# Kernel optimization log

Measured on AMD Instinct MI355X. Metric: run time of the kernel, lower is better.

The kernel has to match this reference:

```python
import jax, jax.numpy as jnp
import numpy as np

N_QUBITS = 10
N_LAYERS = 3
DIM = 2 ** N_QUBITS
N_ANGLES = N_LAYERS * N_QUBITS * 3


def _ring_perm(n):
    """Combined index permutation for the 'ring' CNOT sequence (q0->q1, ..., q_{n-2}->q_{n-1}, q_{n-1}->q0).
    Qubit 0 is the most significant bit, matching bin(i).zfill(n) in the original.
    Each CNOT matrix is a permutation (involution): new_state[j] = old_state[perm[j]]."""
    def cnot_perm(control, target):
        i = np.arange(2 ** n)
        ctrl = (i >> (n - 1 - control)) & 1
        return np.where(ctrl == 1, i ^ (1 << (n - 1 - target)), i)
    total = np.arange(2 ** n)
    pairs = [(q, q + 1) for q in range(n - 1)] + [(n - 1, 0)]
    for c, t in pairs:
        total = total[cnot_perm(c, t)]
    return jnp.asarray(total)

_RING = _ring_perm(N_QUBITS)


def _single_qubit_rot(angles):
    """angles: (S, n_qubits, 3) real -> (S, n_qubits, 2, 2) complex64 Rot(phi, theta, omega)."""
    phi, theta, omega = angles[..., 0], angles[..., 1], angles[..., 2]
    ct = jnp.cos(theta / 2)
    st = jnp.sin(theta / 2)
    ppo = (phi + omega) / 2
    pmo = (phi - omega) / 2
    e_m_ppo = jnp.exp(-1j * ppo)  # complex64
    e_p_ppo = jnp.exp(1j * ppo)
    e_m_pmo = jnp.exp(-1j * pmo)
    e_p_pmo = jnp.exp(1j * pmo)
    m00 = e_m_ppo * ct
    m01 = -e_p_pmo * st
    m10 = e_m_pmo * st
    m11 = e_p_ppo * ct
    S, n = angles.shape[0], angles.shape[1]
    return jnp.stack((m00, m01, m10, m11), axis=2).reshape(S, n, 2, 2)


def _system_unitary(M):
    """Batched Kronecker product over qubits: (S, n, 2, 2) -> (S, 2^n, 2^n).
    Qubit 0 is the most significant index, matching the original einsum string."""
    S = M.shape[0]
    U = M[:, 0]
    d = 2
    for q in range(1, N_QUBITS):
        U = jnp.einsum('aij,akl->aikjl', U, M[:, q]).reshape(S, d * 2, d * 2)
        d *= 2
    return U


def _forward(X, weights, bias):
    S, F = X.shape
    num_reps = N_ANGLES // F + 1
    X_exp = jnp.tile(X, (1, num_reps))[:, :N_ANGLES].reshape(S, N_LAYERS, N_QUBITS, 3)
    angles = X_exp * weights[None] + bias[None]  # (S, L, n, 3)
    state = jnp.zeros((S, DIM), dtype=jnp.complex64).at[:, 0].set(1.0)
    for l in range(N_LAYERS):
        U = _system_unitary(_single_qubit_rot(angles[:, l]))  # (S, 2^n, 2^n)
        state = jnp.einsum('bij,bj->bi', U, state)            # apply Rot layer
        state = state[:, _RING]                               # ring of CNOTs
    return state


def setup_inputs() -> dict:
    key = jax.random.key(0)
    kx, kw, kb = jax.random.split(key, 3)
    X = jax.random.uniform(kx, (32, 20), dtype=jnp.float32)
    weights = jax.random.uniform(kw, (N_LAYERS, N_QUBITS, 3), dtype=jnp.float32)
    bias = jax.random.uniform(kb, (N_LAYERS, N_QUBITS, 3), dtype=jnp.float32)
    return {"X": X, "weights": weights, "bias": bias}


def reference(X, weights, bias):
    return _forward(X, weights, bias)
```

## Files before the change

kernel.cpp:

```cpp
#include <hip/hip_runtime.h>

namespace {

constexpr int NQ   = 10;
constexpr int DIM  = 1024;
constexpr int NL   = 3;
constexpr int FEAT = 20;
constexpr int S    = 32;
constexpr int APL  = 16;

__device__ __forceinline__ float2 gate2(float2 ca, float2 s0, float2 cb, float2 s1) {
    float2 r;
    r.x = ca.x * s0.x - ca.y * s0.y + cb.x * s1.x - cb.y * s1.y;
    r.y = ca.x * s0.y + ca.y * s0.x + cb.x * s1.y + cb.y * s1.x;
    return r;
}

__global__ __launch_bounds__(64) void qsim(const float* __restrict__ X,
                                           const float* __restrict__ W,
                                           const float* __restrict__ Bb,
                                           float* __restrict__ out,
                                           int write_imag)
{
    const int s    = blockIdx.x;
    const int lane = threadIdx.x;

    __shared__ float2 gmat[NL * NQ][4];
    __shared__ float2 pbuf[DIM];

    if (lane < NL * NQ) {
        const int base = lane * 3;
        const float phi   = X[s * FEAT + (base    ) % FEAT] * W[base    ] + Bb[base    ];
        const float theta = X[s * FEAT + (base + 1) % FEAT] * W[base + 1] + Bb[base + 1];
        const float omega = X[s * FEAT + (base + 2) % FEAT] * W[base + 2] + Bb[base + 2];
        float sn, ct;  sincosf(0.5f * theta,         &sn, &ct);
        float sp, cp;  sincosf(0.5f * (phi + omega), &sp, &cp);
        float sm, cm;  sincosf(0.5f * (phi - omega), &sm, &cm);
        gmat[lane][0] = make_float2( cp * ct, -sp * ct);
        gmat[lane][1] = make_float2(-cm * sn, -sm * sn);
        gmat[lane][2] = make_float2( cm * sn, -sm * sn);
        gmat[lane][3] = make_float2( cp * ct,  sp * ct);
    }

    int rsrc[APL];
#pragma unroll
    for (int j = 0; j < APL; ++j) {
        int r = lane * APL + j;
        if (r & 1) r ^= 1 << 9;
#pragma unroll
        for (int c = 8; c >= 0; --c)
            if ((r >> (9 - c)) & 1) r ^= 1 << (8 - c);
        rsrc[j] = r;
    }

    float2 amp[APL];
#pragma unroll
    for (int j = 0; j < APL; ++j) amp[j] = make_float2(0.f, 0.f);
    if (lane == 0) amp[0] = make_float2(1.f, 0.f);

    for (int l = 0; l < NL; ++l) {
        for (int q = 0; q < 6; ++q) {
            const int g = l * NQ + q;
            const float2 m00 = gmat[g][0], m01 = gmat[g][1];
            const float2 m10 = gmat[g][2], m11 = gmat[g][3];
            const int  lb   = 5 - q;
            const int  mask = 1 << lb;
            const bool hi   = (lane >> lb) & 1;
            const float2 ca = hi ? m11 : m00;
            const float2 cb = hi ? m10 : m01;
#pragma unroll
            for (int j = 0; j < APL; ++j) {
                float2 o;
                o.x = __shfl_xor(amp[j].x, mask);
                o.y = __shfl_xor(amp[j].y, mask);
                amp[j] = gate2(ca, amp[j], cb, o);
            }
        }
#pragma unroll
        for (int q = 6; q < 10; ++q) {
            const int g = l * NQ + q;
            const float2 m00 = gmat[g][0], m01 = gmat[g][1];
            const float2 m10 = gmat[g][2], m11 = gmat[g][3];
            const int st = 1 << (9 - q);
#pragma unroll
            for (int p = 0; p < APL; ++p) {
                if (!(p & st)) {
                    const float2 a = amp[p], c = amp[p | st];
                    amp[p]      = gate2(m00, a, m01, c);
                    amp[p | st] = gate2(m10, a, m11, c);
                }
            }
        }
#pragma unroll
        for (int j = 0; j < APL; ++j) pbuf[lane * APL + j] = amp[j];
#pragma unroll
        for (int j = 0; j < APL; ++j) amp[j] = pbuf[rsrc[j]];
    }

    const int base_o = s * DIM + lane * APL;
#pragma unroll
    for (int j = 0; j < APL; ++j) out[base_o + j] = amp[j].x;
    if (write_imag) {
#pragma unroll
        for (int j = 0; j < APL; ++j) out[S * DIM + base_o + j] = amp[j].y;
    }
}

}

extern "C" void kernel_launch(void* const* d_in, const int* in_sizes, int n_in,
                              void* d_out, int out_size, void* d_ws, size_t ws_size,
                              hipStream_t stream) {
    const float* X = (const float*)d_in[0];
    const float* W = (const float*)d_in[1];
    const float* B = (const float*)d_in[2];
    (void)in_sizes; (void)n_in; (void)d_ws; (void)ws_size;
    const int write_imag = (out_size >= 2 * S * DIM) ? 1 : 0;
    qsim<<<S, 64, 0, stream>>>(X, W, B, (float*)d_out, write_imag);
}
```

Baseline: 70.21 us.

## Split each state across four waves and fuse top two qubit gates into 4x4 LDS step

The block grows from one wave to four waves. Each thread now holds 4 amplitudes instead of 16, with a new layout where qubits 0-1 map to wave and register index and qubits 4-9 map to lane bits. Qubits 2-3 are applied within registers, and qubits 4-9 are applied with shuffles. Qubits 0-1 are fused into a precomputed 4x4 matrix that is applied during the LDS gather that also performs the CNOT permutation. This aims to cut the serial per-thread work and raise parallelism, at the cost of extra block barriers and more LDS reads per layer.

```diff
diff --git a/kernel.cpp b/kernel.cpp
--- a/kernel.cpp
+++ b/kernel.cpp
@@ -7,8 +7,16 @@
 constexpr int NL   = 3;
 constexpr int FEAT = 20;
 constexpr int S    = 32;
-constexpr int APL  = 16;
+constexpr int APL  = 4;
 
+__device__ __forceinline__ float2 cmul(float2 a, float2 b) {
+    return make_float2(a.x * b.x - a.y * b.y, a.x * b.y + a.y * b.x);
+}
+__device__ __forceinline__ float2 cmad(float2 a, float2 b, float2 acc) {
+    acc.x += a.x * b.x - a.y * b.y;
+    acc.y += a.x * b.y + a.y * b.x;
+    return acc;
+}
 __device__ __forceinline__ float2 gate2(float2 ca, float2 s0, float2 cb, float2 s1) {
     float2 r;
     r.x = ca.x * s0.x - ca.y * s0.y + cb.x * s1.x - cb.y * s1.y;
@@ -16,93 +24,118 @@
     return r;
 }
 
-__global__ __launch_bounds__(64) void qsim(const float* __restrict__ X,
-                                           const float* __restrict__ W,
-                                           const float* __restrict__ Bb,
-                                           float* __restrict__ out,
-                                           int write_imag)
+__global__ __launch_bounds__(256) void qsim(const float* __restrict__ X,
+                                            const float* __restrict__ W,
+                                            const float* __restrict__ Bb,
+                                            float* __restrict__ out,
+                                            int write_imag)
 {
     const int s    = blockIdx.x;
-    const int lane = threadIdx.x;
+    const int tid  = threadIdx.x;
+    const int wave = tid >> 6;
+    const int lane = tid & 63;
 
     __shared__ float2 gmat[NL * NQ][4];
+    __shared__ float2 M4[NL][16];
     __shared__ float2 pbuf[DIM];
 
-    if (lane < NL * NQ) {
-        const int base = lane * 3;
+    int rlow[APL], rrow[APL];
+#pragma unroll
+    for (int j = 0; j < APL; ++j) {
+        int r = wave * 256 + j * 64 + lane;
+        if (r & 1) r ^= 1 << 9;
+#pragma unroll
+        for (int c = 8; c >= 0; --c)
+            if ((r >> (9 - c)) & 1) r ^= 1 << (8 - c);
+        rlow[j] = r & 255;
+        rrow[j] = r >> 8;
+    }
+
+    if (tid < NL * NQ) {
+        const int base = tid * 3;
         const float phi   = X[s * FEAT + (base    ) % FEAT] * W[base    ] + Bb[base    ];
         const float theta = X[s * FEAT + (base + 1) % FEAT] * W[base + 1] + Bb[base + 1];
         const float omega = X[s * FEAT + (base + 2) % FEAT] * W[base + 2] + Bb[base + 2];
         float sn, ct;  sincosf(0.5f * theta,         &sn, &ct);
         float sp, cp;  sincosf(0.5f * (phi + omega), &sp, &cp);
         float sm, cm;  sincosf(0.5f * (phi - omega), &sm, &cm);
-        gmat[lane][0] = make_float2( cp * ct, -sp * ct);
-        gmat[lane][1] = make_float2(-cm * sn, -sm * sn);
-        gmat[lane][2] = make_float2( cm * sn, -sm * sn);
-        gmat[lane][3] = make_float2( cp * ct,  sp * ct);
+        gmat[tid][0] = make_float2( cp * ct, -sp * ct);
+        gmat[tid][1] = make_float2(-cm * sn, -sm * sn);
+        gmat[tid][2] = make_float2( cm * sn, -sm * sn);
+        gmat[tid][3] = make_float2( cp * ct,  sp * ct);
     }
-
-    int rsrc[APL];
-#pragma unroll
-    for (int j = 0; j < APL; ++j) {
-        int r = lane * APL + j;
-        if (r & 1) r ^= 1 << 9;
-#pragma unroll
-        for (int c = 8; c >= 0; --c)
-            if ((r >> (9 - c)) & 1) r ^= 1 << (8 - c);
-        rsrc[j] = r;
+    if (tid < NL * 16) {
+        const int l = tid >> 4, e = tid & 15, r = e >> 2, k = e & 3;
+        const float2 g0 = gmat[l * NQ + 0][(r >> 1) * 2 + (k >> 1)];
+        const float2 g1 = gmat[l * NQ + 1][(r & 1) * 2 + (k & 1)];
+        M4[l][e] = cmul(g0, g1);
     }
+    __syncthreads();
 
     float2 amp[APL];
 #pragma unroll
     for (int j = 0; j < APL; ++j) amp[j] = make_float2(0.f, 0.f);
-    if (lane == 0) amp[0] = make_float2(1.f, 0.f);
+    if (wave == 0 && lane == 0) amp[0] = make_float2(1.f, 0.f);
 
     for (int l = 0; l < NL; ++l) {
-        for (int q = 0; q < 6; ++q) {
-            const int g = l * NQ + q;
-            const float2 m00 = gmat[g][0], m01 = gmat[g][1];
-            const float2 m10 = gmat[g][2], m11 = gmat[g][3];
-            const int  lb   = 5 - q;
-            const int  mask = 1 << lb;
-            const bool hi   = (lane >> lb) & 1;
-            const float2 ca = hi ? m11 : m00;
-            const float2 cb = hi ? m10 : m01;
+        float2 g[8][4];
+#pragma unroll
+        for (int q = 2; q < 10; ++q) {
+#pragma unroll
+            for (int e = 0; e < 4; ++e) g[q - 2][e] = gmat[l * NQ + q][e];
+        }
+
+#pragma unroll
+        for (int q = 4; q < 10; ++q) {
+            const int  mask = 1 << (9 - q);
+            const bool hi   = (lane & mask) != 0;
+            const float2 ca = hi ? g[q - 2][3] : g[q - 2][0];
+            const float2 cb = hi ? g[q - 2][2] : g[q - 2][1];
+            float2 o[APL];
 #pragma unroll
             for (int j = 0; j < APL; ++j) {
-                float2 o;
-                o.x = __shfl_xor(amp[j].x, mask);
-                o.y = __shfl_xor(amp[j].y, mask);
-                amp[j] = gate2(ca, amp[j], cb, o);
+                o[j].x = __shfl_xor(amp[j].x, mask);
+                o[j].y = __shfl_xor(amp[j].y, mask);
             }
+#pragma unroll
+            for (int j = 0; j < APL; ++j) amp[j] = gate2(ca, amp[j], cb, o[j]);
         }
+
+        {
+            const float2 m00 = g[1][0], m01 = g[1][1], m10 = g[1][2], m11 = g[1][3];
+            float2 a, c;
+            a = amp[0]; c = amp[1]; amp[0] = gate2(m00, a, m01, c); amp[1] = gate2(m10, a, m11, c);
+            a = amp[2]; c = amp[3]; amp[2] = gate2(m00, a, m01, c); amp[3] = gate2(m10, a, m11, c);
+        }
+        {
+            const float2 m00 = g[0][0], m01 = g[0][1], m10 = g[0][2], m11 = g[0][3];
+            float2 a, c;
+            a = amp[0]; c = amp[2]; amp[0] = gate2(m00, a, m01, c); amp[2] = gate2(m10, a, m11, c);
+            a = amp[1]; c = amp[3]; amp[1] = gate2(m00, a, m01, c); amp[3] = gate2(m10, a, m11, c);
+        }
+
+        if (l) __syncthreads();
 #pragma unroll
-        for (int q = 6; q < 10; ++q) {
-            const int g = l * NQ + q;
-            const float2 m00 = gmat[g][0], m01 = gmat[g][1];
-            const float2 m10 = gmat[g][2], m11 = gmat[g][3];
-            const int st = 1 << (9 - q);
+        for (int j = 0; j < APL; ++j)
+            pbuf[wave * 256 + j * 64 + lane] = amp[j];
+        __syncthreads();
 #pragma unroll
-            for (int p = 0; p < APL; ++p) {
-                if (!(p & st)) {
-                    const float2 a = amp[p], c = amp[p | st];
-                    amp[p]      = gate2(m00, a, m01, c);
-                    amp[p | st] = gate2(m10, a, m11, c);
-                }
-            }
+        for (int j = 0; j < APL; ++j) {
+            const float2* Mrow = &M4[l][rrow[j] * 4];
+            float2 acc = make_float2(0.f, 0.f);
+#pragma unroll
+            for (int k = 0; k < 4; ++k)
+                acc = cmad(Mrow[k], pbuf[rlow[j] + (k << 8)], acc);
+            amp[j] = acc;
         }
-#pragma unroll
-        for (int j = 0; j < APL; ++j) pbuf[lane * APL + j] = amp[j];
-#pragma unroll
-        for (int j = 0; j < APL; ++j) amp[j] = pbuf[rsrc[j]];
     }
 
-    const int base_o = s * DIM + lane * APL;
+    const int base_o = s * DIM + wave * 256 + lane;
 #pragma unroll
-    for (int j = 0; j < APL; ++j) out[base_o + j] = amp[j].x;
+    for (int j = 0; j < APL; ++j) out[base_o + j * 64] = amp[j].x;
     if (write_imag) {
 #pragma unroll
-        for (int j = 0; j < APL; ++j) out[S * DIM + base_o + j] = amp[j].y;
+        for (int j = 0; j < APL; ++j) out[S * DIM + base_o + j * 64] = amp[j].y;
     }
 }
 
@@ -116,5 +149,5 @@
     const float* B = (const float*)d_in[2];
     (void)in_sizes; (void)n_in; (void)d_ws; (void)ws_size;
     const int write_imag = (out_size >= 2 * S * DIM) ? 1 : 0;
-    qsim<<<S, 64, 0, stream>>>(X, W, B, (float*)d_out, write_imag);
+    qsim<<<S, 256, 0, stream>>>(X, W, B, (float*)d_out, write_imag);
 }
```

Result: faster. 62.14 us (-11.5%).
